# Optimization experiments

Hardware: AMD Instinct MI355X
Metric: run time of the kernel (lower is better)

## Reference

```python
import jax, jax.numpy as jnp
import numpy as np

EMBED = 1024
HEADS = 16
HEAD_DIM = EMBED // HEADS
EPS = 1e-5


def setup_inputs() -> dict:
    key = jax.random.key(0)
    ks = jax.random.split(key, 5)
    s = 1.0 / np.sqrt(EMBED)
    return {
        "x": jax.random.normal(ks[0], (2, 2048, EMBED), dtype=jnp.float32),
        "Wq": jax.random.normal(ks[1], (EMBED, EMBED), dtype=jnp.float32) * s,
        "Wk": jax.random.normal(ks[2], (EMBED, EMBED), dtype=jnp.float32) * s,
        "Wv": jax.random.normal(ks[3], (EMBED, EMBED), dtype=jnp.float32) * s,
        "Wout": jax.random.normal(ks[4], (EMBED, EMBED), dtype=jnp.float32) * s,
        "gamma": jnp.ones((EMBED,), dtype=jnp.float32),
        "beta": jnp.zeros((EMBED,), dtype=jnp.float32),
    }


def reference(x, Wq, Wk, Wv, Wout, gamma, beta):
    B, S, E = x.shape
    # nn.Linear(bias=False): y = x @ W.T; weight stored as [out, in]
    q = (x @ Wq.T).reshape(B, S, HEADS, HEAD_DIM)
    k = (x @ Wk.T).reshape(B, S, HEADS, HEAD_DIM)
    v = (x @ Wv.T).reshape(B, S, HEADS, HEAD_DIM)
    scale = 1.0 / jnp.sqrt(jnp.float32(HEAD_DIM)).astype(x.dtype)
    scores = jnp.einsum("bqhd,bkhd->bhqk", q, k) * scale  # [B,H,S,S]
    probs = jax.nn.softmax(scores, axis=-1)
    attn = jnp.einsum("bhqk,bkhd->bqhd", probs, v).reshape(B, S, E)
    out = attn @ Wout.T
    y = out + x
    mu = jnp.mean(y, axis=-1, keepdims=True)
    var = jnp.var(y, axis=-1, keepdims=True)
    return (y - mu) * jax.lax.rsqrt(var + EPS) * gamma + beta
```

## Files before the change

### kernel.cpp

```cpp
#include <hip/hip_runtime.h>
#include <hip/hip_bf16.h>
#include <cstdint>
#include <cstddef>

#define SEQ   2048
#define BATCH 2
#define NROWS 4096
#define EMB   1024
#define NHEAD 16
#define HD    64
#define KVBLK 64

typedef __attribute__((ext_vector_type(8))) short bf16x8;
typedef __attribute__((ext_vector_type(4))) float f32x4;
typedef __attribute__((ext_vector_type(16))) float f32x16;
typedef __attribute__((ext_vector_type(2))) int i32x2;
typedef __hip_bfloat16 bf16_t;

__device__ __forceinline__ int swz(int row, int cb) { return cb ^ ((row & 7) << 4); }

__device__ __forceinline__ void plswap(int a, int b, int& ra, int& rb) {
#if __has_builtin(__builtin_amdgcn_permlane32_swap)
  i32x2 r = __builtin_amdgcn_permlane32_swap(a, b, false, false);
  ra = r[0]; rb = r[1];
#else
  const int pa = __shfl_xor(a, 32), pb = __shfl_xor(b, 32);
  const bool lo = (threadIdx.x & 63) < 32;
  ra = lo ? a : pb;
  rb = lo ? pa : b;
#endif
}
__device__ __forceinline__ float pairmax32(float v) {
  int r0, r1;
  plswap(__float_as_int(v), __float_as_int(v), r0, r1);
  return fmaxf(__int_as_float(r0), __int_as_float(r1));
}
__device__ __forceinline__ float pairsum32(float v) {
  int r0, r1;
  plswap(__float_as_int(v), __float_as_int(v), r0, r1);
  return __int_as_float(r0) + __int_as_float(r1);
}

__global__ __launch_bounds__(256) void cast_f32_to_bf16(const float* __restrict__ in,
                                                        bf16_t* __restrict__ out, int n4) {
  int i = blockIdx.x * 256 + threadIdx.x;
  if (i >= n4) return;
  float4 v = reinterpret_cast<const float4*>(in)[i];
  union { ushort4 u; bf16_t h[4]; } o;
  o.h[0] = __float2bfloat16(v.x);
  o.h[1] = __float2bfloat16(v.y);
  o.h[2] = __float2bfloat16(v.z);
  o.h[3] = __float2bfloat16(v.w);
  reinterpret_cast<ushort4*>(out)[i] = o.u;
}

__global__ __launch_bounds__(256) void cast4_w(const float* __restrict__ a,
                                               const float* __restrict__ b,
                                               const float* __restrict__ c,
                                               const float* __restrict__ d,
                                               bf16_t* __restrict__ oa, bf16_t* __restrict__ ob,
                                               bf16_t* __restrict__ oc, bf16_t* __restrict__ od,
                                               int n4) {
  const int z = blockIdx.z;
  const float* in = (z == 0) ? a : (z == 1) ? b : (z == 2) ? c : d;
  bf16_t* out = (z == 0) ? oa : (z == 1) ? ob : (z == 2) ? oc : od;
  int i = blockIdx.x * 256 + threadIdx.x;
  if (i >= n4) return;
  float4 v = reinterpret_cast<const float4*>(in)[i];
  union { ushort4 u; bf16_t h[4]; } o;
  o.h[0] = __float2bfloat16(v.x);
  o.h[1] = __float2bfloat16(v.y);
  o.h[2] = __float2bfloat16(v.z);
  o.h[3] = __float2bfloat16(v.w);
  reinterpret_cast<ushort4*>(out)[i] = o.u;
}

template <int MODE>
__device__ __forceinline__ void gemm128_body(const bf16_t* __restrict__ A,
                                             const bf16_t* __restrict__ W,
                                             bf16_t* __restrict__ Ob,
                                             float* __restrict__ Of,
                                             const float* __restrict__ Res) {
  __shared__ __align__(16) bf16_t As[128 * 32];
  __shared__ __align__(16) bf16_t Bs[128 * 32];
  const int tid = threadIdx.x;
  const int lane = tid & 63;
  const int wv = tid >> 6;
  const int wm = wv >> 1, wn = wv & 1;
  const int brow = blockIdx.y * 128;
  const int bcol = blockIdx.x * 128;
  const int lr = lane & 15, lg = lane >> 4;

  f32x4 acc[4][4] = {};

  auto* As3 = (__attribute__((address_space(3))) char*)As;
  auto* Bs3 = (__attribute__((address_space(3))) char*)Bs;

  for (int k0 = 0; k0 < EMB; k0 += 32) {
    __syncthreads();
#pragma unroll
    for (int i = 0; i < 2; ++i) {
      const int chunk = i * 256 + tid;
      const int row = chunk >> 2;
      const int kc = (chunk & 3) * 8;
      const bf16_t* ga = A + (size_t)(brow + row) * EMB + k0 + kc;
      const bf16_t* gb = W + (size_t)(bcol + row) * EMB + k0 + kc;
      __builtin_amdgcn_global_load_lds((const __attribute__((address_space(1))) void*)ga,
                                       (__attribute__((address_space(3))) void*)(As3 + chunk * 16),
                                       16, 0, 0);
      __builtin_amdgcn_global_load_lds((const __attribute__((address_space(1))) void*)gb,
                                       (__attribute__((address_space(3))) void*)(Bs3 + chunk * 16),
                                       16, 0, 0);
    }
    __syncthreads();

    bf16x8 af[4], bfr[4];
#pragma unroll
    for (int m = 0; m < 4; ++m)
      af[m] = *reinterpret_cast<const bf16x8*>(&As[(wm * 64 + m * 16 + lr) * 32 + lg * 8]);
#pragma unroll
    for (int n = 0; n < 4; ++n)
      bfr[n] = *reinterpret_cast<const bf16x8*>(&Bs[(wn * 64 + n * 16 + lr) * 32 + lg * 8]);
#pragma unroll
    for (int m = 0; m < 4; ++m)
#pragma unroll
      for (int n = 0; n < 4; ++n)
        acc[m][n] = __builtin_amdgcn_mfma_f32_16x16x32_bf16(af[m], bfr[n], acc[m][n], 0, 0, 0);
  }

  const int r0 = brow + wm * 64;
  const int c0 = bcol + wn * 64;
#pragma unroll
  for (int m = 0; m < 4; ++m)
#pragma unroll
    for (int n = 0; n < 4; ++n) {
      if (MODE == 2) {
        const int row0 = r0 + m * 16 + lg * 4;
        const int col = c0 + n * 16 + lr;
        const size_t vt_row = (size_t)(row0 >> 11) * 1024 + col;
        const int s = row0 & 2047;
        union { uint2 u2; bf16_t h[4]; } pu;
#pragma unroll
        for (int r = 0; r < 4; ++r) pu.h[r] = __float2bfloat16(acc[m][n][r]);
        *reinterpret_cast<uint2*>(Ob + vt_row * SEQ + s) = pu.u2;
      } else {
#pragma unroll
        for (int r = 0; r < 4; ++r) {
          const int row = r0 + m * 16 + lg * 4 + r;
          const int col = c0 + n * 16 + lr;
          const size_t idx = (size_t)row * EMB + col;
          if (MODE == 0) Ob[idx] = __float2bfloat16(acc[m][n][r]);
          else Of[idx] = acc[m][n][r] + Res[idx];
        }
      }
    }
}

__global__ __launch_bounds__(256) void gemm_qkv(const bf16_t* __restrict__ X,
                                                const bf16_t* __restrict__ Wq,
                                                const bf16_t* __restrict__ Wk,
                                                const bf16_t* __restrict__ Wv,
                                                bf16_t* __restrict__ Q,
                                                bf16_t* __restrict__ K,
                                                bf16_t* __restrict__ Vt) {
  if (blockIdx.z == 0)      gemm128_body<0>(X, Wq, Q, nullptr, nullptr);
  else if (blockIdx.z == 1) gemm128_body<0>(X, Wk, K, nullptr, nullptr);
  else                      gemm128_body<2>(X, Wv, Vt, nullptr, nullptr);
}

__global__ __launch_bounds__(256) void gemm_out(const bf16_t* __restrict__ Attn,
                                                const bf16_t* __restrict__ Wo,
                                                float* __restrict__ Y,
                                                const float* __restrict__ X) {
  gemm128_body<1>(Attn, Wo, nullptr, Y, X);
}

__global__ __launch_bounds__(256) void attn_kernel(const bf16_t* __restrict__ Q,
                                                   const bf16_t* __restrict__ K,
                                                   const bf16_t* __restrict__ Vt,
                                                   bf16_t* __restrict__ Oout) {
  __shared__ __align__(16) bf16_t Ks[2][KVBLK * 64];
  __shared__ __align__(16) bf16_t Vs[2][64 * KVBLK];

  const int tid = threadIdx.x;
  const int lane = tid & 63;
  const int wv = tid >> 6;
  const int lq = lane & 31;
  const int lh = lane >> 5;

  const int f = blockIdx.x + 16 * blockIdx.y + 256 * blockIdx.z;
  const int w = (f & 7) * 64 + (f >> 3);
  const int qb = w & 15;
  const int h = (w >> 4) & 15;
  const int b = w >> 8;

  const size_t baseRow = (size_t)b * SEQ;
  const int hoff = h * HD;
  const int q0 = qb * 128 + wv * 32;

  const float qscale = 0.125f * 1.44269504f;
  bf16x8 qf[4];
#pragma unroll
  for (int ks = 0; ks < 4; ++ks) {
    bf16x8 t = *reinterpret_cast<const bf16x8*>(
        &Q[(baseRow + q0 + lq) * EMB + hoff + ks * 16 + lh * 8]);
    union { bf16x8 v; bf16_t h[8]; } u;
    u.v = t;
#pragma unroll
    for (int e = 0; e < 8; ++e)
      u.h[e] = __float2bfloat16(__bfloat162float(u.h[e]) * qscale);
    qf[ks] = u.v;
  }

  f32x16 o[2] = {};
  float mrow = -1e30f, lrow = 0.f;

  auto* Ks3 = (__attribute__((address_space(3))) char*)&Ks[0][0];
  auto* Vs3 = (__attribute__((address_space(3))) char*)&Vs[0][0];

  const int srow = tid >> 3;
  const int scb = swz(srow, (tid & 7) * 16) >> 1;
  const bf16_t* kp = K + (baseRow + srow) * EMB + hoff + scb;
  const bf16_t* vp = Vt + ((size_t)(b * 1024 + hoff) + srow) * SEQ + scb;

  auto stage = [&](int buf, const bf16_t* kpp, const bf16_t* vpp) {
#pragma unroll
    for (int i = 0; i < 2; ++i) {
      const int c = i * 256 + tid;
      __builtin_amdgcn_global_load_lds(
          (const __attribute__((address_space(1))) void*)(kpp + i * 32 * EMB),
          (__attribute__((address_space(3))) void*)(Ks3 + buf * 8192 + c * 16), 16, 0, 0);
      __builtin_amdgcn_global_load_lds(
          (const __attribute__((address_space(1))) void*)(vpp + i * 32 * SEQ),
          (__attribute__((address_space(3))) void*)(Vs3 + buf * 8192 + c * 16), 16, 0, 0);
    }
  };

  stage(0, kp, vp);
  kp += KVBLK * EMB;
  vp += KVBLK;
  __syncthreads();

  for (int it = 0; it < SEQ / KVBLK; ++it) {
    const int cur = it & 1;
    if (it + 1 < SEQ / KVBLK) {
      stage(cur ^ 1, kp, vp);
      kp += KVBLK * EMB;
      vp += KVBLK;
    }

    const char* Kb = (const char*)Ks + cur * 8192;
    const char* Vb = (const char*)Vs + cur * 8192;

    f32x16 st[2] = {};
    __builtin_amdgcn_s_setprio(1);
#pragma unroll
    for (int jh = 0; jh < 2; ++jh) {
      const int row = jh * 32 + lq;
#pragma unroll
      for (int ks = 0; ks < 4; ++ks) {
        bf16x8 kf = *reinterpret_cast<const bf16x8*>(Kb + row * 128 + swz(lq, ks * 32 + lh * 16));
        st[jh] = __builtin_amdgcn_mfma_f32_32x32x16_bf16(kf, qf[ks], st[jh], 0, 0, 0);
      }
    }
    __builtin_amdgcn_s_setprio(0);

    float mx = -1e30f;
#pragma unroll
    for (int jh = 0; jh < 2; ++jh)
#pragma unroll
      for (int r = 0; r < 16; ++r) mx = fmaxf(mx, st[jh][r]);
    mx = pairmax32(mx);

    if (!__all(mx - mrow <= 8.f)) {
      const float mnew = fmaxf(mrow, mx);
      const float al = __builtin_amdgcn_exp2f(mrow - mnew);
      mrow = mnew;
      lrow *= al;
#pragma unroll
      for (int jh = 0; jh < 2; ++jh)
#pragma unroll
        for (int r = 0; r < 16; ++r) o[jh][r] *= al;
    }

    float lsp[2];
#pragma unroll
    for (int jh = 0; jh < 2; ++jh) {
#pragma unroll
      for (int r = 0; r < 16; ++r) st[jh][r] = __builtin_amdgcn_exp2f(st[jh][r] - mrow);
      float a0 = (st[jh][0] + st[jh][1]) + (st[jh][2] + st[jh][3]);
      float a1 = (st[jh][4] + st[jh][5]) + (st[jh][6] + st[jh][7]);
      float a2 = (st[jh][8] + st[jh][9]) + (st[jh][10] + st[jh][11]);
      float a3 = (st[jh][12] + st[jh][13]) + (st[jh][14] + st[jh][15]);
      lsp[jh] = (a0 + a1) + (a2 + a3);
    }
    lrow += pairsum32(lsp[0] + lsp[1]);

    bf16x8 pb[4];
#pragma unroll
    for (int jh = 0; jh < 2; ++jh)
#pragma unroll
      for (int sub = 0; sub < 2; ++sub) {
        int w01, w23, w45, w67;
        asm("v_cvt_pk_bf16_f32 %0, %1, %2" : "=v"(w01) : "v"(st[jh][sub * 8 + 0]), "v"(st[jh][sub * 8 + 1]));
        asm("v_cvt_pk_bf16_f32 %0, %1, %2" : "=v"(w23) : "v"(st[jh][sub * 8 + 2]), "v"(st[jh][sub * 8 + 3]));
        asm("v_cvt_pk_bf16_f32 %0, %1, %2" : "=v"(w45) : "v"(st[jh][sub * 8 + 4]), "v"(st[jh][sub * 8 + 5]));
        asm("v_cvt_pk_bf16_f32 %0, %1, %2" : "=v"(w67) : "v"(st[jh][sub * 8 + 6]), "v"(st[jh][sub * 8 + 7]));
        int d0, d1, d2, d3;
        plswap(w01, w45, d0, d2);
        plswap(w23, w67, d1, d3);
        union { int i[4]; bf16x8 v; } u;
        u.i[0] = d0; u.i[1] = d1; u.i[2] = d2; u.i[3] = d3;
        pb[jh * 2 + sub] = u.v;
      }

    __builtin_amdgcn_s_setprio(1);
#pragma unroll
    for (int dh = 0; dh < 2; ++dh) {
      const int row = dh * 32 + lq;
#pragma unroll
      for (int js = 0; js < 4; ++js) {
        bf16x8 vf = *reinterpret_cast<const bf16x8*>(Vb + row * 128 + swz(lq, js * 32 + lh * 16));
        o[dh] = __builtin_amdgcn_mfma_f32_32x32x16_bf16(vf, pb[js], o[dh], 0, 0, 0);
      }
    }
    __builtin_amdgcn_s_setprio(0);

    __syncthreads();
  }

  const float inv = 1.f / lrow;
  const size_t orow = (baseRow + q0 + lq) * EMB + hoff;
#pragma unroll
  for (int dh = 0; dh < 2; ++dh)
#pragma unroll
    for (int g = 0; g < 4; ++g) {
      union { uint2 u2; bf16_t h[4]; } pu;
#pragma unroll
      for (int r = 0; r < 4; ++r) pu.h[r] = __float2bfloat16(o[dh][g * 4 + r] * inv);
      *reinterpret_cast<uint2*>(Oout + orow + dh * 32 + g * 8 + lh * 4) = pu.u2;
    }
}

__global__ __launch_bounds__(256) void ln_kernel(const float* __restrict__ Y,
                                                 const float* __restrict__ gamma,
                                                 const float* __restrict__ beta,
                                                 float* __restrict__ Out) {
  const int row = blockIdx.x;
  const int tid = threadIdx.x;
  const float4 v = reinterpret_cast<const float4*>(Y + (size_t)row * EMB)[tid];
  float s = v.x + v.y + v.z + v.w;
  float s2 = v.x * v.x + v.y * v.y + v.z * v.z + v.w * v.w;
#pragma unroll
  for (int m = 1; m < 64; m <<= 1) {
    s += __shfl_xor(s, m);
    s2 += __shfl_xor(s2, m);
  }
  __shared__ float ws[4], ws2[4];
  const int w = tid >> 6;
  if ((tid & 63) == 0) { ws[w] = s; ws2[w] = s2; }
  __syncthreads();
  s = ws[0] + ws[1] + ws[2] + ws[3];
  s2 = ws2[0] + ws2[1] + ws2[2] + ws2[3];
  const float mu = s * (1.f / EMB);
  const float var = s2 * (1.f / EMB) - mu * mu;
  const float rstd = rsqrtf(var + 1e-5f);
  const float4 g = reinterpret_cast<const float4*>(gamma)[tid];
  const float4 bt = reinterpret_cast<const float4*>(beta)[tid];
  float4 ov;
  ov.x = (v.x - mu) * rstd * g.x + bt.x;
  ov.y = (v.y - mu) * rstd * g.y + bt.y;
  ov.z = (v.z - mu) * rstd * g.z + bt.z;
  ov.w = (v.w - mu) * rstd * g.w + bt.w;
  reinterpret_cast<float4*>(Out + (size_t)row * EMB)[tid] = ov;
}

extern "C" void kernel_launch(void* const* d_in, const int* in_sizes, int n_in,
                              void* d_out, int out_size, void* d_ws, size_t ws_size,
                              hipStream_t stream) {
  const float* x = (const float*)d_in[0];
  const float* Wq = (const float*)d_in[1];
  const float* Wk = (const float*)d_in[2];
  const float* Wv = (const float*)d_in[3];
  const float* Wo = (const float*)d_in[4];
  const float* gamma = (const float*)d_in[5];
  const float* beta = (const float*)d_in[6];
  float* out = (float*)d_out;

  char* p = (char*)d_ws;
  const size_t sz_rows_bf = (size_t)NROWS * EMB * sizeof(bf16_t);
  const size_t sz_w_bf = (size_t)EMB * EMB * sizeof(bf16_t);
  bf16_t* xb = (bf16_t*)p; p += sz_rows_bf;
  bf16_t* wqb = (bf16_t*)p; p += sz_w_bf;
  bf16_t* wkb = (bf16_t*)p; p += sz_w_bf;
  bf16_t* wvb = (bf16_t*)p; p += sz_w_bf;
  bf16_t* wob = (bf16_t*)p; p += sz_w_bf;
  bf16_t* q = (bf16_t*)p; p += sz_rows_bf;
  bf16_t* k = (bf16_t*)p; p += sz_rows_bf;
  bf16_t* vt = (bf16_t*)p; p += sz_rows_bf;
  bf16_t* attn = (bf16_t*)p; p += sz_rows_bf;
  float* y = (float*)q;

  const int n4x = NROWS * EMB / 4;
  const int n4w = EMB * EMB / 4;
  cast_f32_to_bf16<<<n4x / 256, 256, 0, stream>>>(x, xb, n4x);
  cast4_w<<<dim3(n4w / 256, 1, 4), 256, 0, stream>>>(Wq, Wk, Wv, Wo, wqb, wkb, wvb, wob, n4w);

  gemm_qkv<<<dim3(EMB / 128, NROWS / 128, 3), 256, 0, stream>>>(xb, wqb, wkb, wvb, q, k, vt);

  attn_kernel<<<dim3(SEQ / 128, NHEAD, BATCH), 256, 0, stream>>>(q, k, vt, attn);

  gemm_out<<<dim3(EMB / 128, NROWS / 128, 1), 256, 0, stream>>>(attn, wob, y, x);

  ln_kernel<<<NROWS, 256, 0, stream>>>(y, gamma, beta, out);
}
```

Before: 133.9 us.

## Software-pipeline attention loop with triple-buffered KV and overlapped QK^T/softmax

Restructures the attention inner loop into a two-stage software pipeline. The QK^T MFMAs for the next KV tile are issued before the softmax and PV of the previous tile, with a third LDS buffer so prefetch, score compute and finalisation use different tiles. The aim is to overlap the exp/reduction VALU work with matrix-core work and hide LDS load latency. The cost is more LDS (three K/V buffers) and more live accumulator registers, which may reduce occupancy.

```diff
diff --git a/kernel.cpp b/kernel.cpp
--- a/kernel.cpp
+++ b/kernel.cpp
@@ -10,6 +10,7 @@
 #define NHEAD 16
 #define HD    64
 #define KVBLK 64
+#define NT    (SEQ / KVBLK)
 
 typedef __attribute__((ext_vector_type(8))) short bf16x8;
 typedef __attribute__((ext_vector_type(4))) float f32x4;
@@ -179,8 +180,8 @@
                                                    const bf16_t* __restrict__ K,
                                                    const bf16_t* __restrict__ Vt,
                                                    bf16_t* __restrict__ Oout) {
-  __shared__ __align__(16) bf16_t Ks[2][KVBLK * 64];
-  __shared__ __align__(16) bf16_t Vs[2][64 * KVBLK];
+  __shared__ __align__(16) bf16_t Ks[3][KVBLK * 64];
+  __shared__ __align__(16) bf16_t Vs[3][KVBLK * 64];
 
   const int tid = threadIdx.x;
   const int lane = tid & 63;
@@ -212,7 +213,7 @@
     qf[ks] = u.v;
   }
 
-  f32x16 o[2] = {};
+  f32x16 o0 = {}, o1 = {};
   float mrow = -1e30f, lrow = 0.f;
 
   auto* Ks3 = (__attribute__((address_space(3))) char*)&Ks[0][0];
@@ -223,53 +224,46 @@
   const bf16_t* kp = K + (baseRow + srow) * EMB + hoff + scb;
   const bf16_t* vp = Vt + ((size_t)(b * 1024 + hoff) + srow) * SEQ + scb;
 
-  auto stage = [&](int buf, const bf16_t* kpp, const bf16_t* vpp) {
+  auto stage = [&](int buf) {
 #pragma unroll
     for (int i = 0; i < 2; ++i) {
       const int c = i * 256 + tid;
       __builtin_amdgcn_global_load_lds(
-          (const __attribute__((address_space(1))) void*)(kpp + i * 32 * EMB),
+          (const __attribute__((address_space(1))) void*)(kp + i * 32 * EMB),
           (__attribute__((address_space(3))) void*)(Ks3 + buf * 8192 + c * 16), 16, 0, 0);
       __builtin_amdgcn_global_load_lds(
-          (const __attribute__((address_space(1))) void*)(vpp + i * 32 * SEQ),
+          (const __attribute__((address_space(1))) void*)(vp + i * 32 * SEQ),
           (__attribute__((address_space(3))) void*)(Vs3 + buf * 8192 + c * 16), 16, 0, 0);
     }
+    kp += KVBLK * EMB;
+    vp += KVBLK;
   };
 
-  stage(0, kp, vp);
-  kp += KVBLK * EMB;
-  vp += KVBLK;
-  __syncthreads();
-
-  for (int it = 0; it < SEQ / KVBLK; ++it) {
-    const int cur = it & 1;
-    if (it + 1 < SEQ / KVBLK) {
-      stage(cur ^ 1, kp, vp);
-      kp += KVBLK * EMB;
-      vp += KVBLK;
-    }
-
-    const char* Kb = (const char*)Ks + cur * 8192;
-    const char* Vb = (const char*)Vs + cur * 8192;
-
-    f32x16 st[2] = {};
+  auto QKT = [&](int buf, f32x16& s0, f32x16& s1) {
+    const char* Kb = (const char*)Ks + buf * 8192;
+    s0 = (f32x16){};
+    s1 = (f32x16){};
     __builtin_amdgcn_s_setprio(1);
 #pragma unroll
-    for (int jh = 0; jh < 2; ++jh) {
-      const int row = jh * 32 + lq;
-#pragma unroll
-      for (int ks = 0; ks < 4; ++ks) {
-        bf16x8 kf = *reinterpret_cast<const bf16x8*>(Kb + row * 128 + swz(lq, ks * 32 + lh * 16));
-        st[jh] = __builtin_amdgcn_mfma_f32_32x32x16_bf16(kf, qf[ks], st[jh], 0, 0, 0);
-      }
+    for (int ks = 0; ks < 4; ++ks) {
+      bf16x8 kf0 = *reinterpret_cast<const bf16x8*>(Kb + lq * 128 + swz(lq, ks * 32 + lh * 16));
+      s0 = __builtin_amdgcn_mfma_f32_32x32x16_bf16(kf0, qf[ks], s0, 0, 0, 0);
+    }
+#pragma unroll
+    for (int ks = 0; ks < 4; ++ks) {
+      bf16x8 kf1 = *reinterpret_cast<const bf16x8*>(Kb + (32 + lq) * 128 + swz(lq, ks * 32 + lh * 16));
+      s1 = __builtin_amdgcn_mfma_f32_32x32x16_bf16(kf1, qf[ks], s1, 0, 0, 0);
     }
     __builtin_amdgcn_s_setprio(0);
-
+  };
+
+  auto FIN = [&](f32x16& st0, f32x16& st1, int buf) {
+    const char* Vb = (const char*)Vs + buf * 8192;
     float mx = -1e30f;
 #pragma unroll
-    for (int jh = 0; jh < 2; ++jh)
-#pragma unroll
-      for (int r = 0; r < 16; ++r) mx = fmaxf(mx, st[jh][r]);
+    for (int r = 0; r < 16; ++r) mx = fmaxf(mx, st0[r]);
+#pragma unroll
+    for (int r = 0; r < 16; ++r) mx = fmaxf(mx, st1[r]);
     mx = pairmax32(mx);
 
     if (!__all(mx - mrow <= 8.f)) {
@@ -278,34 +272,38 @@
       mrow = mnew;
       lrow *= al;
 #pragma unroll
-      for (int jh = 0; jh < 2; ++jh)
-#pragma unroll
-        for (int r = 0; r < 16; ++r) o[jh][r] *= al;
-    }
-
-    float lsp[2];
-#pragma unroll
-    for (int jh = 0; jh < 2; ++jh) {
-#pragma unroll
-      for (int r = 0; r < 16; ++r) st[jh][r] = __builtin_amdgcn_exp2f(st[jh][r] - mrow);
-      float a0 = (st[jh][0] + st[jh][1]) + (st[jh][2] + st[jh][3]);
-      float a1 = (st[jh][4] + st[jh][5]) + (st[jh][6] + st[jh][7]);
-      float a2 = (st[jh][8] + st[jh][9]) + (st[jh][10] + st[jh][11]);
-      float a3 = (st[jh][12] + st[jh][13]) + (st[jh][14] + st[jh][15]);
-      lsp[jh] = (a0 + a1) + (a2 + a3);
-    }
-    lrow += pairsum32(lsp[0] + lsp[1]);
+      for (int r = 0; r < 16; ++r) o0[r] *= al;
+#pragma unroll
+      for (int r = 0; r < 16; ++r) o1[r] *= al;
+    }
+
+#pragma unroll
+    for (int r = 0; r < 16; ++r) st0[r] = __builtin_amdgcn_exp2f(st0[r] - mrow);
+#pragma unroll
+    for (int r = 0; r < 16; ++r) st1[r] = __builtin_amdgcn_exp2f(st1[r] - mrow);
+    {
+      float a0 = (st0[0] + st0[1]) + (st0[2] + st0[3]);
+      float a1 = (st0[4] + st0[5]) + (st0[6] + st0[7]);
+      float a2 = (st0[8] + st0[9]) + (st0[10] + st0[11]);
+      float a3 = (st0[12] + st0[13]) + (st0[14] + st0[15]);
+      float b0 = (st1[0] + st1[1]) + (st1[2] + st1[3]);
+      float b1 = (st1[4] + st1[5]) + (st1[6] + st1[7]);
+      float b2 = (st1[8] + st1[9]) + (st1[10] + st1[11]);
+      float b3 = (st1[12] + st1[13]) + (st1[14] + st1[15]);
+      lrow += pairsum32(((a0 + a1) + (a2 + a3)) + ((b0 + b1) + (b2 + b3)));
+    }
 
     bf16x8 pb[4];
 #pragma unroll
     for (int jh = 0; jh < 2; ++jh)
 #pragma unroll
       for (int sub = 0; sub < 2; ++sub) {
+        const f32x16& s = jh ? st1 : st0;
         int w01, w23, w45, w67;
-        asm("v_cvt_pk_bf16_f32 %0, %1, %2" : "=v"(w01) : "v"(st[jh][sub * 8 + 0]), "v"(st[jh][sub * 8 + 1]));
-        asm("v_cvt_pk_bf16_f32 %0, %1, %2" : "=v"(w23) : "v"(st[jh][sub * 8 + 2]), "v"(st[jh][sub * 8 + 3]));
-        asm("v_cvt_pk_bf16_f32 %0, %1, %2" : "=v"(w45) : "v"(st[jh][sub * 8 + 4]), "v"(st[jh][sub * 8 + 5]));
-        asm("v_cvt_pk_bf16_f32 %0, %1, %2" : "=v"(w67) : "v"(st[jh][sub * 8 + 6]), "v"(st[jh][sub * 8 + 7]));
+        asm("v_cvt_pk_bf16_f32 %0, %1, %2" : "=v"(w01) : "v"(s[sub * 8 + 0]), "v"(s[sub * 8 + 1]));
+        asm("v_cvt_pk_bf16_f32 %0, %1, %2" : "=v"(w23) : "v"(s[sub * 8 + 2]), "v"(s[sub * 8 + 3]));
+        asm("v_cvt_pk_bf16_f32 %0, %1, %2" : "=v"(w45) : "v"(s[sub * 8 + 4]), "v"(s[sub * 8 + 5]));
+        asm("v_cvt_pk_bf16_f32 %0, %1, %2" : "=v"(w67) : "v"(s[sub * 8 + 6]), "v"(s[sub * 8 + 7]));
         int d0, d1, d2, d3;
         plswap(w01, w45, d0, d2);
         plswap(w23, w67, d1, d3);
@@ -316,30 +314,56 @@
 
     __builtin_amdgcn_s_setprio(1);
 #pragma unroll
-    for (int dh = 0; dh < 2; ++dh) {
-      const int row = dh * 32 + lq;
-#pragma unroll
-      for (int js = 0; js < 4; ++js) {
-        bf16x8 vf = *reinterpret_cast<const bf16x8*>(Vb + row * 128 + swz(lq, js * 32 + lh * 16));
-        o[dh] = __builtin_amdgcn_mfma_f32_32x32x16_bf16(vf, pb[js], o[dh], 0, 0, 0);
-      }
+    for (int js = 0; js < 4; ++js) {
+      bf16x8 vf0 = *reinterpret_cast<const bf16x8*>(Vb + lq * 128 + swz(lq, js * 32 + lh * 16));
+      o0 = __builtin_amdgcn_mfma_f32_32x32x16_bf16(vf0, pb[js], o0, 0, 0, 0);
+    }
+#pragma unroll
+    for (int js = 0; js < 4; ++js) {
+      bf16x8 vf1 = *reinterpret_cast<const bf16x8*>(Vb + (32 + lq) * 128 + swz(lq, js * 32 + lh * 16));
+      o1 = __builtin_amdgcn_mfma_f32_32x32x16_bf16(vf1, pb[js], o1, 0, 0, 0);
     }
     __builtin_amdgcn_s_setprio(0);
-
+  };
+
+  f32x16 sA0, sA1, sB0, sB1;
+
+  stage(0);
+  __syncthreads();
+  stage(1);
+  QKT(0, sA0, sA1);
+
+  for (int t = 1; t + 1 < NT; t += 2) {
     __syncthreads();
-  }
+    stage((t + 1) % 3);
+    QKT(t % 3, sB0, sB1);
+    FIN(sA0, sA1, (t - 1) % 3);
+    __syncthreads();
+    if (t + 2 < NT) stage((t + 2) % 3);
+    QKT((t + 1) % 3, sA0, sA1);
+    FIN(sB0, sB1, t % 3);
+  }
+  __syncthreads();
+  QKT((NT - 1) % 3, sB0, sB1);
+  FIN(sA0, sA1, (NT - 2) % 3);
+  FIN(sB0, sB1, (NT - 1) % 3);
 
   const float inv = 1.f / lrow;
   const size_t orow = (baseRow + q0 + lq) * EMB + hoff;
 #pragma unroll
-  for (int dh = 0; dh < 2; ++dh)
-#pragma unroll
-    for (int g = 0; g < 4; ++g) {
-      union { uint2 u2; bf16_t h[4]; } pu;
-#pragma unroll
-      for (int r = 0; r < 4; ++r) pu.h[r] = __float2bfloat16(o[dh][g * 4 + r] * inv);
-      *reinterpret_cast<uint2*>(Oout + orow + dh * 32 + g * 8 + lh * 4) = pu.u2;
-    }
+  for (int g = 0; g < 4; ++g) {
+    union { uint2 u2; bf16_t h[4]; } pu;
+#pragma unroll
+    for (int r = 0; r < 4; ++r) pu.h[r] = __float2bfloat16(o0[g * 4 + r] * inv);
+    *reinterpret_cast<uint2*>(Oout + orow + g * 8 + lh * 4) = pu.u2;
+  }
+#pragma unroll
+  for (int g = 0; g < 4; ++g) {
+    union { uint2 u2; bf16_t h[4]; } pu;
+#pragma unroll
+    for (int r = 0; r < 4; ++r) pu.h[r] = __float2bfloat16(o1[g * 4 + r] * inv);
+    *reinterpret_cast<uint2*>(Oout + orow + 32 + g * 8 + lh * 4) = pu.u2;
+  }
 }
 
 __global__ __launch_bounds__(256) void ln_kernel(const float* __restrict__ Y,
```

After: 128.8 us. 1.04x faster.
